# Kernel optimization log

Hardware: AMD Instinct MI355X
Metric: run time of the kernel (lower is better)

Reference implementation:

```python
import jax, jax.numpy as jnp
import numpy as np

B, D, G, H = 65536, 512, 16, 128


def setup_inputs() -> dict:
    key = jax.random.key(0)
    ks = jax.random.split(key, 8)
    s = 1.0 / np.sqrt(D)
    sh = 1.0 / np.sqrt(H)
    return {
        "z": jax.random.normal(ks[0], (B, D), dtype=jnp.float32),
        "Wc": jax.random.uniform(ks[1], (D, G), jnp.float32, -s, s),
        "bc": jax.random.uniform(ks[2], (G,), jnp.float32, -s, s),
        "W1": jax.random.uniform(ks[3], (G, D, H), jnp.float32, -s, s),
        "b1": jax.random.uniform(ks[4], (G, H), jnp.float32, -s, s),
        "W2": jax.random.uniform(ks[5], (G, H), jnp.float32, -sh, sh),
        "b2": jax.random.uniform(ks[6], (G,), jnp.float32, -sh, sh),
    }


def reference(z, Wc, bc, W1, b1, W2, b2):
    # classifier head + softmax
    logits = z @ Wc + bc                                  # [B, G]
    p_g = jax.nn.softmax(logits, axis=1)                  # [B, G]
    # G experts fused as one batched GEMM: fc1 -> GELU -> fc2 (dropout = identity at eval)
    h = jax.nn.gelu(jnp.einsum('bd,gdh->bgh', z, W1) + b1, approximate=False)  # [B, G, H]
    y_all = jnp.einsum('bgh,gh->bg', h, W2) + b2          # [B, G]
    return logits, p_g, y_all
```

## Files before the change

### kernel.cpp

```cpp
#include <hip/hip_runtime.h>
#include <cstdint>
#include <cstddef>

typedef __bf16 bf16x8 __attribute__((ext_vector_type(8)));
typedef float f32x4 __attribute__((ext_vector_type(4)));
typedef unsigned short ushortx8 __attribute__((ext_vector_type(8)));

__device__ __forceinline__ unsigned short f2bf(float f) {
  union { float f; unsigned int u; } v; v.f = f;
  return (unsigned short)((v.u + 0x8000u) >> 16);
}

__device__ __forceinline__ float gelu_s(float x) {
  float x2 = x * x;
  float p = __builtin_fmaf(x2, -0.10294324f, -2.30220819f);
  float e = __builtin_amdgcn_exp2f(x * p);
  return x * __builtin_amdgcn_rcpf(1.0f + e);
}

#define GLOAD16(gsrc, ldst)                                                  \
  __builtin_amdgcn_global_load_lds(                                          \
      (const __attribute__((address_space(1))) unsigned int*)(gsrc),         \
      (__attribute__((address_space(3))) unsigned int*)(uintptr_t)(          \
          (char*)(ldst)),                                                    \
      16, 0, 0)

#define SWZ_FRAG(base, R, C8)                                                \
  (*(const bf16x8*)((base) + (((R) >> 5) * 4096) +                           \
                    ((((R)&31) * 8 + ((C8) ^ ((R)&7))) * 16)))

__device__ __forceinline__ void stage_A_f32(const float* __restrict__ ag,
                                            char* lds, int tid, int ko) {
  f32x4 a0[4], a1[4];
#pragma unroll
  for (int it = 0; it < 4; ++it) {
    const float* p = ag + it * 32 * 512 + ko;
    a0[it] = *(const f32x4*)(p);
    a1[it] = *(const f32x4*)(p + 4);
  }
#pragma unroll
  for (int it = 0; it < 4; ++it) {
    ushortx8 r;
    r[0] = f2bf(a0[it][0]); r[1] = f2bf(a0[it][1]);
    r[2] = f2bf(a0[it][2]); r[3] = f2bf(a0[it][3]);
    r[4] = f2bf(a1[it][0]); r[5] = f2bf(a1[it][1]);
    r[6] = f2bf(a1[it][2]); r[7] = f2bf(a1[it][3]);
    *(ushortx8*)(lds + it * 4096 + tid * 16) = r;
  }
}

__device__ __forceinline__ void expert_tile(
    int e, int mbase, const float* __restrict__ z,
    const unsigned short* __restrict__ w1t, const float* __restrict__ b1,
    const float* __restrict__ w2, const float* __restrict__ b2,
    float* __restrict__ out, char* lds, int tid, int wq, int l15, int l4,
    int c8s) {
  char* ldsB = lds + 16384;
  const float* ag = z + (size_t)(mbase + (tid >> 3)) * 512 + c8s;
  const unsigned short* bg = w1t + e * 65536 + (tid >> 3) * 512 + c8s;
  const int wr = wq >> 1;
  const int wc = wq & 1;
  f32x4 acc[4][4] = {};
  for (int kt = 0; kt < 8; ++kt) {
    const int ko = kt * 64;
#pragma unroll
    for (int it = 0; it < 4; ++it)
      GLOAD16(bg + it * 32 * 512 + ko, ldsB + it * 4096 + tid * 16);
    stage_A_f32(ag, lds, tid, ko);
    __syncthreads();
#pragma unroll
    for (int ks = 0; ks < 2; ++ks) {
      bf16x8 af[4];
#pragma unroll
      for (int rt = 0; rt < 4; ++rt)
        af[rt] = SWZ_FRAG(lds, wr * 64 + rt * 16 + l15, ks * 4 + l4);
#pragma unroll
      for (int ct = 0; ct < 4; ++ct) {
        bf16x8 bfv = SWZ_FRAG(ldsB, wc * 64 + ct * 16 + l15, ks * 4 + l4);
#pragma unroll
        for (int rt = 0; rt < 4; ++rt)
          acc[rt][ct] = __builtin_amdgcn_mfma_f32_16x16x32_bf16(
              af[rt], bfv, acc[rt][ct], 0, 0, 0);
      }
    }
    __syncthreads();
  }
  float b1v[4], w2v[4];
#pragma unroll
  for (int ct = 0; ct < 4; ++ct) {
    int n = wc * 64 + ct * 16 + l15;
    b1v[ct] = b1[e * 128 + n];
    w2v[ct] = w2[e * 128 + n];
  }
  float* ylds = (float*)(lds + 32768);
#pragma unroll
  for (int rt = 0; rt < 4; ++rt) {
#pragma unroll
    for (int i = 0; i < 4; ++i) {
      float s = 0.0f;
#pragma unroll
      for (int ct = 0; ct < 4; ++ct)
        s += gelu_s(acc[rt][ct][i] + b1v[ct]) * w2v[ct];
#pragma unroll
      for (int off = 1; off < 16; off <<= 1) s += __shfl_xor(s, off, 16);
      if (l15 == 0) ylds[wq * 64 + rt * 16 + l4 * 4 + i] = s;
    }
  }
  __syncthreads();
  if (tid < 128) {
    int rl = tid & 63, half = tid >> 6;
    float y = ylds[half * 128 + rl] + ylds[half * 128 + 64 + rl] + b2[e];
    out[(size_t)2097152 + (size_t)(mbase + half * 64 + rl) * 16 + e] = y;
  }
}

__device__ __forceinline__ void logits_tile(
    int mbase, const float* __restrict__ z,
    const unsigned short* __restrict__ wct, const float* __restrict__ bc,
    float* __restrict__ out, char* lds, int tid, int wq, int l15, int l4,
    int c8s) {
  const float* ag = z + (size_t)(mbase + (tid >> 3)) * 512 + c8s;
  const unsigned short* wb = wct + l15 * 512 + l4 * 8;
  f32x4 acc2[2] = {};
  for (int kt = 0; kt < 8; ++kt) {
    const int ko = kt * 64;
    stage_A_f32(ag, lds, tid, ko);
    bf16x8 bfr0 = *(const bf16x8*)(wb + ko);
    bf16x8 bfr1 = *(const bf16x8*)(wb + ko + 32);
    __syncthreads();
#pragma unroll
    for (int rt = 0; rt < 2; ++rt) {
      bf16x8 a0 = SWZ_FRAG(lds, wq * 32 + rt * 16 + l15, l4);
      acc2[rt] =
          __builtin_amdgcn_mfma_f32_16x16x32_bf16(a0, bfr0, acc2[rt], 0, 0, 0);
      bf16x8 a1 = SWZ_FRAG(lds, wq * 32 + rt * 16 + l15, 4 + l4);
      acc2[rt] =
          __builtin_amdgcn_mfma_f32_16x16x32_bf16(a1, bfr1, acc2[rt], 0, 0, 0);
    }
    __syncthreads();
  }
  float bcv = bc[l15];
#pragma unroll
  for (int rt = 0; rt < 2; ++rt) {
#pragma unroll
    for (int i = 0; i < 4; ++i) {
      int row = wq * 32 + rt * 16 + l4 * 4 + i;
      float lg = acc2[rt][i] + bcv;
      float mx = lg;
#pragma unroll
      for (int off = 1; off < 16; off <<= 1)
        mx = fmaxf(mx, __shfl_xor(mx, off, 16));
      float ex = __expf(lg - mx);
      float sm = ex;
#pragma unroll
      for (int off = 1; off < 16; off <<= 1) sm += __shfl_xor(sm, off, 16);
      size_t ro = (size_t)(mbase + row) * 16 + l15;
      out[ro] = lg;
      out[1048576 + ro] = ex / sm;
    }
  }
}

__global__ __launch_bounds__(256) void k_convert(
    const float* __restrict__ W1, const float* __restrict__ Wc,
    unsigned short* __restrict__ w1t, unsigned short* __restrict__ wct) {
  int bid = blockIdx.x;
  int tid = threadIdx.x;
  if (bid < 1024) {
    __shared__ float tile[32][33];
    int gg = bid >> 6;
    int t = bid & 63;
    int d0 = (t >> 2) * 32;
    int h0 = (t & 3) * 32;
    int tx = tid & 31, ty = tid >> 5;
#pragma unroll
    for (int r = 0; r < 4; ++r)
      tile[r * 8 + ty][tx] = W1[(gg << 16) + (d0 + r * 8 + ty) * 128 + h0 + tx];
    __syncthreads();
#pragma unroll
    for (int r = 0; r < 4; ++r)
      w1t[(gg << 16) + (h0 + r * 8 + ty) * 512 + d0 + tx] =
          f2bf(tile[tx][r * 8 + ty]);
  } else {
#pragma unroll
    for (int j = 0; j < 32; ++j) {
      int i = j * 256 + tid;
      wct[(i & 15) * 512 + (i >> 4)] = f2bf(Wc[i]);
    }
  }
}

__global__ __launch_bounds__(256, 4) void k_main(
    const float* __restrict__ z, const unsigned short* __restrict__ w1t,
    const unsigned short* __restrict__ wct, const float* __restrict__ bc,
    const float* __restrict__ b1, const float* __restrict__ w2,
    const float* __restrict__ b2, float* __restrict__ out) {
  __shared__ alignas(16) char lds[33792];
  const int tid = threadIdx.x;
  const int wq = tid >> 6;
  const int l15 = tid & 15;
  const int l4 = (tid >> 4) & 3;
  const int c8s = (((tid & 7) ^ ((tid >> 3) & 7))) * 8;
  const int xcd = blockIdx.x & 7;
  const int t = blockIdx.x >> 3;
  const int pl = t / 17;
  const int r = t - pl * 17;
  const int mbase = (xcd * 64 + pl) * 128;
  if (r == 0) {
    logits_tile(mbase, z, wct, bc, out, lds, tid, wq, l15, l4, c8s);
  } else {
    expert_tile(r - 1, mbase, z, w1t, b1, w2, b2, out, lds, tid, wq, l15, l4,
                c8s);
  }
}

extern "C" void kernel_launch(void* const* d_in, const int* in_sizes, int n_in,
                              void* d_out, int out_size, void* d_ws,
                              size_t ws_size, hipStream_t stream) {
  const float* z = (const float*)d_in[0];
  const float* Wc = (const float*)d_in[1];
  const float* bc = (const float*)d_in[2];
  const float* W1 = (const float*)d_in[3];
  const float* b1 = (const float*)d_in[4];
  const float* W2 = (const float*)d_in[5];
  const float* b2 = (const float*)d_in[6];
  float* out = (float*)d_out;

  unsigned short* w1t = (unsigned short*)d_ws;
  unsigned short* wct = w1t + (size_t)16 * 128 * 512;

  k_convert<<<1024 + 1, 256, 0, stream>>>(W1, Wc, w1t, wct);
  k_main<<<8 * 1088, 256, 0, stream>>>(z, w1t, wct, bc, b1, W2, b2, out);
}
```

Baseline: 353.6 us.

## Fuse weight conversion and main compute into one persistent cooperative kernel

Replaces the two-kernel sequence (weight transpose/convert, then main GEMM) with a single cooperative persistent kernel. Blocks first convert W1 and Wc to bf16, then meet at a grid-wide barrier, then loop over the output tiles in a grid-stride fashion. The aim is to remove one kernel launch and the gap between the two kernels. In exchange it adds a grid sync and host-side occupancy queries on every call. The persistent grid is capped at 1024 blocks and may schedule tiles less evenly than the original 8704-block launch.

```diff
diff --git a/kernel.cpp b/kernel.cpp
--- a/kernel.cpp
+++ b/kernel.cpp
@@ -1,6 +1,9 @@
 #include <hip/hip_runtime.h>
+#include <hip/hip_cooperative_groups.h>
 #include <cstdint>
 #include <cstddef>
+
+namespace cg = cooperative_groups;
 
 typedef __bf16 bf16x8 __attribute__((ext_vector_type(8)));
 typedef float f32x4 __attribute__((ext_vector_type(4)));
@@ -158,6 +161,63 @@
       out[ro] = lg;
       out[1048576 + ro] = ex / sm;
     }
+  }
+}
+
+__global__ __launch_bounds__(256, 4) void k_coop(
+    const float* __restrict__ z, const float* __restrict__ W1,
+    const float* __restrict__ Wc, const float* __restrict__ bc,
+    const float* __restrict__ b1, const float* __restrict__ w2,
+    const float* __restrict__ b2, unsigned short* __restrict__ w1t,
+    unsigned short* __restrict__ wct, float* __restrict__ out) {
+  __shared__ alignas(16) char lds[33792];
+  const int NB = gridDim.x;
+  const int p = blockIdx.x;
+  const int tid = threadIdx.x;
+
+  for (int j = p; j < 1056; j += NB) {
+    if (j < 1024) {
+      float* tile = (float*)lds;
+      int gg = j >> 6;
+      int t6 = j & 63;
+      int d0 = (t6 >> 2) * 32;
+      int h0 = (t6 & 3) * 32;
+      int tx = tid & 31, ty = tid >> 5;
+#pragma unroll
+      for (int r = 0; r < 4; ++r)
+        tile[(r * 8 + ty) * 33 + tx] =
+            W1[(gg << 16) + (d0 + r * 8 + ty) * 128 + h0 + tx];
+      __syncthreads();
+#pragma unroll
+      for (int r = 0; r < 4; ++r)
+        w1t[(gg << 16) + (h0 + r * 8 + ty) * 512 + d0 + tx] =
+            f2bf(tile[tx * 33 + r * 8 + ty]);
+      __syncthreads();
+    } else {
+      int i = (j - 1024) * 256 + tid;
+      wct[(i & 15) * 512 + (i >> 4)] = f2bf(Wc[i]);
+    }
+  }
+
+  __threadfence();
+  cg::this_grid().sync();
+  __threadfence();
+
+  const int wq = tid >> 6;
+  const int l15 = tid & 15;
+  const int l4 = (tid >> 4) & 3;
+  const int c8s = (((tid & 7) ^ ((tid >> 3) & 7))) * 8;
+  for (int v = p; v < 8704; v += NB) {
+    const int xcd = v & 7;
+    const int t = v >> 3;
+    const int pl = t / 17;
+    const int r = t - pl * 17;
+    const int mbase = (xcd * 64 + pl) * 128;
+    if (r == 0)
+      logits_tile(mbase, z, wct, bc, out, lds, tid, wq, l15, l4, c8s);
+    else
+      expert_tile(r - 1, mbase, z, w1t, b1, w2, b2, out, lds, tid, wq, l15,
+                  l4, c8s);
   }
 }
 
@@ -206,12 +266,11 @@
   const int pl = t / 17;
   const int r = t - pl * 17;
   const int mbase = (xcd * 64 + pl) * 128;
-  if (r == 0) {
+  if (r == 0)
     logits_tile(mbase, z, wct, bc, out, lds, tid, wq, l15, l4, c8s);
-  } else {
+  else
     expert_tile(r - 1, mbase, z, w1t, b1, w2, b2, out, lds, tid, wq, l15, l4,
                 c8s);
-  }
 }
 
 extern "C" void kernel_launch(void* const* d_in, const int* in_sizes, int n_in,
@@ -229,6 +288,30 @@
   unsigned short* w1t = (unsigned short*)d_ws;
   unsigned short* wct = w1t + (size_t)16 * 128 * 512;
 
-  k_convert<<<1024 + 1, 256, 0, stream>>>(W1, Wc, w1t, wct);
-  k_main<<<8 * 1088, 256, 0, stream>>>(z, w1t, wct, bc, b1, W2, b2, out);
-}
+  int dev = 0;
+  (void)hipGetDevice(&dev);
+  int coop = 0;
+  (void)hipDeviceGetAttribute(&coop, hipDeviceAttributeCooperativeLaunch, dev);
+  int ncu = 0;
+  (void)hipDeviceGetAttribute(&ncu, hipDeviceAttributeMultiprocessorCount,
+                              dev);
+  int maxb = 0;
+  (void)hipOccupancyMaxActiveBlocksPerMultiprocessor(&maxb, k_coop, 256, 0);
+  int NB = maxb * (ncu > 0 ? ncu : 256);
+  if (NB > 1024) NB = 1024;
+  NB &= ~7;
+
+  bool ok = false;
+  if (coop && NB >= 8) {
+    void* kargs[] = {(void*)&z,  (void*)&W1,  (void*)&Wc,  (void*)&bc,
+                     (void*)&b1, (void*)&W2,  (void*)&b2,  (void*)&w1t,
+                     (void*)&wct, (void*)&out};
+    hipError_t err = hipLaunchCooperativeKernel(
+        (const void*)k_coop, dim3(NB), dim3(256), kargs, 0, stream);
+    ok = (err == hipSuccess);
+  }
+  if (!ok) {
+    k_convert<<<1024 + 1, 256, 0, stream>>>(W1, Wc, w1t, wct);
+    k_main<<<8 * 1088, 256, 0, stream>>>(z, w1t, wct, bc, b1, W2, b2, out);
+  }
+}
```

New measurement: 579.4 us. +63.8%, slower.
